# Performance work log

Hardware: AMD Instinct MI355X
Metric: run time of the kernel (lower is better)

Reference implementation:

```python
import jax, jax.numpy as jnp
import numpy as np

B, C, H, W = 16, 16, 256, 256
HID, OUT_C, IN_C = 128, 13, 3

_SOBEL_X = np.array([[-1, 0, 1], [-2, 0, 2], [-1, 0, 1]], dtype=np.float32)
_SOBEL_Y = _SOBEL_X.T


def setup_inputs() -> dict:
    key = jax.random.key(0)
    k1, k2, k3, k4 = jax.random.split(key, 4)
    return {
        "input_grid": jax.random.normal(k1, (B, C, H, W), dtype=jnp.float32),
        "w1": jax.random.normal(k2, (HID, 3 * C), dtype=jnp.float32) * 0.0001,
        "b1": jax.random.normal(k3, (HID,), dtype=jnp.float32) * 0.0001,
        "w2": jax.random.normal(k4, (OUT_C, HID), dtype=jnp.float32) * 0.0001,
    }


def _depthwise_sobel(x_padded, filt2d):
    # x_padded: [B, C, H+2, W+2]; depthwise 3x3 valid conv (groups=C)
    c = x_padded.shape[1]
    kern = jnp.broadcast_to(jnp.asarray(filt2d)[None, None], (c, 1, 3, 3))
    return jax.lax.conv_general_dilated(
        x_padded, kern, window_strides=(1, 1), padding="VALID",
        feature_group_count=c,
        dimension_numbers=("NCHW", "OIHW", "NCHW"))


def reference(input_grid, w1, b1, w2):
    # circular pad by 1 on spatial dims
    xp = jnp.pad(input_grid, ((0, 0), (0, 0), (1, 1), (1, 1)), mode="wrap")
    gx = _depthwise_sobel(xp, _SOBEL_X)
    gy = _depthwise_sobel(xp, _SOBEL_Y)
    # perception grid: [B, 3C, H, W]
    perception = jnp.concatenate([input_grid, gx, gy], axis=1)
    # update network: 1x1 conv -> ReLU -> 1x1 conv (dropout = identity in eval)
    h = jax.nn.relu(jnp.einsum("bchw,oc->bohw", perception, w1)
                    + b1[None, :, None, None])
    ds = jnp.einsum("bchw,oc->bohw", h, w2)  # [B, C-IN_C, H, W]
    # residual add to channels 3: of the state
    return input_grid.at[:, IN_C:].add(ds)
```

## Files before the change

### kernel.cpp

```cpp
#include <hip/hip_runtime.h>

#define BB   16
#define CC   16
#define HH   256
#define WW   256
#define HID  128
#define OUTC 13

typedef short short8 __attribute__((ext_vector_type(8)));
typedef float floatx16 __attribute__((ext_vector_type(16)));

__device__ __forceinline__ unsigned short f2bf(float x) {
    unsigned int u = __float_as_uint(x);
    u += 0x7fffu + ((u >> 16) & 1u);
    return (unsigned short)(u >> 16);
}

#define W1F_BYTES 36864
#define W2F_OFF   36864

__global__ __launch_bounds__(256) void gca_prep(
    const float* __restrict__ w1, const float* __restrict__ w2,
    unsigned char* __restrict__ ws)
{
    const int id = blockIdx.x * 256 + threadIdx.x;
    const float SX[9] = {-1.f, 0.f, 1.f, -2.f, 0.f, 2.f, -1.f, 0.f, 1.f};
    const float SY[9] = {-1.f, -2.f, -1.f, 0.f, 0.f, 0.f, 1.f, 2.f, 1.f};

    if (id < 2304) {
        const int mtG  = id / 576;
        const int rem  = id % 576;
        const int tap  = rem / 64;
        const int lane = rem % 64;
        const int p  = lane & 31, hi = lane >> 5;
        const int hid = 32 * mtG + p;
        const float cen = (tap == 4) ? 1.f : 0.f;
        const float sxv = SX[tap], syv = SY[tap];
        const float* wr = w1 + hid * 48;
        unsigned int o[4];
        for (int k = 0; k < 4; ++k) {
            int c0 = 8 * hi + 2 * k;
            float v0 = wr[c0]     * cen + wr[16 + c0]     * sxv + wr[32 + c0]     * syv;
            float v1 = wr[c0 + 1] * cen + wr[16 + c0 + 1] * sxv + wr[32 + c0 + 1] * syv;
            o[k] = (unsigned int)f2bf(v0) | ((unsigned int)f2bf(v1) << 16);
        }
        *(uint4*)(ws + (size_t)id * 16) = make_uint4(o[0], o[1], o[2], o[3]);
    } else if (id < 2816) {
        const int id2 = id - 2304;
        const int s    = id2 / 64;
        const int lane = id2 % 64;
        const int outc = lane & 31, hi = lane >> 5;
        unsigned int o[4];
        for (int k = 0; k < 4; ++k) {
            int hid0 = 16 * s + 8 * hi + 2 * k;
            float v0 = (outc < OUTC) ? w2[outc * HID + hid0]     : 0.f;
            float v1 = (outc < OUTC) ? w2[outc * HID + hid0 + 1] : 0.f;
            o[k] = (unsigned int)f2bf(v0) | ((unsigned int)f2bf(v1) << 16);
        }
        *(uint4*)(ws + W2F_OFF + (size_t)id2 * 16) = make_uint4(o[0], o[1], o[2], o[3]);
    }
}

#define TILE_DW 6120
#define CBUF_DW 2304

__global__ __launch_bounds__(256) void gca_main(
    const float* __restrict__ in,
    const float* __restrict__ b1,
    const unsigned char* __restrict__ ws,
    float* __restrict__ out)
{
    __shared__ unsigned int lds[TILE_DW + CBUF_DW];

    const int tid  = threadIdx.x;
    const int wid  = tid >> 6;
    const int lane = tid & 63;
    const int hw   = wid & 1;
    const int P    = wid >> 1;
    const int p    = lane & 31;
    const int hi   = lane >> 5;

    const int bI = blockIdx.x >> 7;
    const int rm = blockIdx.x & 127;
    const int y0 = (rm >> 3) << 4;
    const int x0 = (rm & 7)  << 5;

    {
        unsigned short* tus = (unsigned short*)lds;
        const float* inb = in + ((size_t)bI << 20);
        for (int i = tid; i < 16 * 18 * 34; i += 256) {
            int c   = i / 612;
            int rem = i % 612;
            int row = rem / 34;
            int col = rem % 34;
            int y = (y0 + row - 1) & 255;
            int x = (x0 + col - 1) & 255;
            float v = inb[(c << 16) + (y << 8) + x];
            tus[(row * 34 + col) * 20 + c] = f2bf(v);
        }
    }
    __syncthreads();

    const unsigned char* w1f = ws + ((size_t)(2 * hw) * 9) * 64 * 16;
    const unsigned char* w2f = ws + W2F_OFF + (size_t)(4 * hw) * 64 * 16;
    const int cb = TILE_DW + P * (64 * 18) + lane * 18;

#pragma unroll 1
    for (int t = 0; t < 8; ++t) {
        const int row = y0 + 2 * t + P;

        floatx16 acc1[2];
#pragma unroll
        for (int m = 0; m < 2; ++m) {
            const int hb = 64 * hw + 32 * m + 4 * hi;
#pragma unroll
            for (int rr = 0; rr < 4; ++rr) {
                float4 bv = *(const float4*)(b1 + hb + 8 * rr);
                acc1[m][4 * rr + 0] = bv.x;
                acc1[m][4 * rr + 1] = bv.y;
                acc1[m][4 * rr + 2] = bv.z;
                acc1[m][4 * rr + 3] = bv.w;
            }
        }

#pragma unroll
        for (int tap = 0; tap < 9; ++tap) {
            const int tr  = 2 * t + P + tap / 3;
            const int col = p + tap % 3;
            const int dwo = (tr * 34 + col) * 10 + 4 * hi;
            union { unsigned int u[4]; short8 s; } bfr;
            uint2 lo2 = *(const uint2*)&lds[dwo];
            uint2 hi2 = *(const uint2*)&lds[dwo + 2];
            bfr.u[0] = lo2.x; bfr.u[1] = lo2.y; bfr.u[2] = hi2.x; bfr.u[3] = hi2.y;
#pragma unroll
            for (int m = 0; m < 2; ++m) {
                short8 af = *(const short8*)(w1f + (size_t)((m * 9 + tap) * 64 + lane) * 16);
                acc1[m] = __builtin_amdgcn_mfma_f32_32x32x16_bf16(af, bfr.s, acc1[m], 0, 0, 0);
            }
        }

        uint2 hrun[8];
#pragma unroll
        for (int m = 0; m < 2; ++m)
#pragma unroll
            for (int rr = 0; rr < 4; ++rr) {
                float h0 = fmaxf(acc1[m][4 * rr + 0], 0.f);
                float h1 = fmaxf(acc1[m][4 * rr + 1], 0.f);
                float h2 = fmaxf(acc1[m][4 * rr + 2], 0.f);
                float h3 = fmaxf(acc1[m][4 * rr + 3], 0.f);
                hrun[4 * m + rr].x = (unsigned int)f2bf(h0) | ((unsigned int)f2bf(h1) << 16);
                hrun[4 * m + rr].y = (unsigned int)f2bf(h2) | ((unsigned int)f2bf(h3) << 16);
            }

        floatx16 acc2 = {};
#pragma unroll
        for (int sp = 0; sp < 4; ++sp) {
            uint2 r0 = hrun[2 * sp];
            uint2 r1 = hrun[2 * sp + 1];
            uint2 x0s, x1s;
            x0s.x = (unsigned int)__shfl_xor((int)r0.x, 32);
            x0s.y = (unsigned int)__shfl_xor((int)r0.y, 32);
            x1s.x = (unsigned int)__shfl_xor((int)r1.x, 32);
            x1s.y = (unsigned int)__shfl_xor((int)r1.y, 32);
            union { unsigned int u[4]; short8 s; } b2;
            uint2 lo = hi ? x1s : r0;
            uint2 hg = hi ? r1  : x0s;
            b2.u[0] = lo.x; b2.u[1] = lo.y; b2.u[2] = hg.x; b2.u[3] = hg.y;
            short8 a2 = *(const short8*)(w2f + (size_t)(sp * 64 + lane) * 16);
            acc2 = __builtin_amdgcn_mfma_f32_32x32x16_bf16(a2, b2.s, acc2, 0, 0, 0);
        }

        if (hw == 1) {
#pragma unroll
            for (int k = 0; k < 8; ++k) {
                uint2 v;
                v.x = __float_as_uint(acc2[2 * k]);
                v.y = __float_as_uint(acc2[2 * k + 1]);
                *(uint2*)&lds[cb + 2 * k] = v;
            }
        }
        __syncthreads();

        if (hw == 0) {
#pragma unroll
            for (int r = 0; r < 16; ++r) {
                int outc = (r & 3) + 8 * (r >> 2) + 4 * hi;
                if (outc < OUTC) {
                    float sum = acc2[r] + __uint_as_float(lds[cb + r]);
                    int idx = ((bI * 16 + 3 + outc) << 16) + (row << 8) + x0 + p;
                    out[idx] = in[idx] + sum;
                }
            }
        } else {
#pragma unroll
            for (int k = 0; k < 2; ++k) {
                int e = lane + 64 * k;
                if (e < 96) {
                    int c  = e >> 5;
                    int px = e & 31;
                    int idx = ((bI * 16 + c) << 16) + (row << 8) + x0 + px;
                    out[idx] = in[idx];
                }
            }
        }
        __syncthreads();
    }
}

extern "C" void kernel_launch(void* const* d_in, const int* in_sizes, int n_in,
                              void* d_out, int out_size, void* d_ws, size_t ws_size,
                              hipStream_t stream) {
    const float* x  = (const float*)d_in[0];
    const float* w1 = (const float*)d_in[1];
    const float* b1 = (const float*)d_in[2];
    const float* w2 = (const float*)d_in[3];
    float* out = (float*)d_out;
    unsigned char* ws = (unsigned char*)d_ws;

    hipLaunchKernelGGL(gca_prep, dim3(11), dim3(256), 0, stream, w1, w2, ws);
    hipLaunchKernelGGL(gca_main, dim3(2048), dim3(256), 0, stream, x, b1, ws, out);
}
```

Before: 214.2 us.

## Halve block tile to 8 rows with 2 waves and vectorize bf16 tile loading

Each block now handles 8 output rows with 128 threads (two waves, one per hidden half) instead of 16 rows with four waves. This halves LDS per block and doubles the grid, aiming for more resident blocks and better latency hiding. The halo tile load drops its per-element div/mod and 16-bit scattered LDS stores. Instead each thread loads coalesced rows for four channels and writes packed bf16 pairs as 32-bit words. The trade-off is a larger halo fraction (10 loaded rows per 8 output rows) and more per-block setup.

```diff
diff --git a/kernel.cpp b/kernel.cpp
--- a/kernel.cpp
+++ b/kernel.cpp
@@ -14,6 +14,9 @@
     unsigned int u = __float_as_uint(x);
     u += 0x7fffu + ((u >> 16) & 1u);
     return (unsigned short)(u >> 16);
+}
+__device__ __forceinline__ unsigned int pack2(float lo, float hi) {
+    return (unsigned int)f2bf(lo) | ((unsigned int)f2bf(hi) << 16);
 }
 
 #define W1F_BYTES 36864
@@ -61,53 +64,68 @@
     }
 }
 
-#define TILE_DW 6120
-#define CBUF_DW 2304
-
-__global__ __launch_bounds__(256) void gca_main(
+#define TILE_DW 3400
+#define CBUF_DW 1152
+#define LDS_DW  (TILE_DW + CBUF_DW)
+
+__global__ __launch_bounds__(128) void gca_main(
     const float* __restrict__ in,
     const float* __restrict__ b1,
     const unsigned char* __restrict__ ws,
     float* __restrict__ out)
 {
-    __shared__ unsigned int lds[TILE_DW + CBUF_DW];
+    __shared__ unsigned int lds[LDS_DW];
 
     const int tid  = threadIdx.x;
     const int wid  = tid >> 6;
     const int lane = tid & 63;
-    const int hw   = wid & 1;
-    const int P    = wid >> 1;
+    const int hw   = wid;
     const int p    = lane & 31;
     const int hi   = lane >> 5;
 
-    const int bI = blockIdx.x >> 7;
-    const int rm = blockIdx.x & 127;
-    const int y0 = (rm >> 3) << 4;
+    const int bI = blockIdx.x >> 8;
+    const int rm = blockIdx.x & 255;
+    const int y0 = (rm >> 3) << 3;
     const int x0 = (rm & 7)  << 5;
 
+    const float* inb  = in  + ((size_t)bI << 20);
+    float*       outb = out + ((size_t)bI << 20);
+
     {
-        unsigned short* tus = (unsigned short*)lds;
-        const float* inb = in + ((size_t)bI << 20);
-        for (int i = tid; i < 16 * 18 * 34; i += 256) {
-            int c   = i / 612;
-            int rem = i % 612;
-            int row = rem / 34;
-            int col = rem % 34;
-            int y = (y0 + row - 1) & 255;
-            int x = (x0 + col - 1) & 255;
-            float v = inb[(c << 16) + (y << 8) + x];
-            tus[(row * 34 + col) * 20 + c] = f2bf(v);
+        const int g = tid >> 5, l = tid & 31;
+        const float* cp0 = inb + ((size_t)(2 * g) << 16);
+        const int xA = (x0 + l - 1) & 255;
+        const int xB = (x0 + l + 31) & 255;
+        const int ldsA = l * 10 + g;
+        const int ldsB = (l + 32) * 10 + g;
+        const bool doB = (l < 2);
+        for (int rw = 0; rw < 10; ++rw) {
+            const int yo = ((y0 + rw - 1) & 255) << 8;
+            float a0 = cp0[yo + xA];
+            float a1 = cp0[yo + xA + (1 << 16)];
+            float b0 = cp0[yo + xA + (8 << 16)];
+            float b1v = cp0[yo + xA + (9 << 16)];
+            lds[rw * 340 + ldsA]     = pack2(a0, a1);
+            lds[rw * 340 + ldsA + 4] = pack2(b0, b1v);
+            if (doB) {
+                float c0 = cp0[yo + xB];
+                float c1 = cp0[yo + xB + (1 << 16)];
+                float d0 = cp0[yo + xB + (8 << 16)];
+                float d1 = cp0[yo + xB + (9 << 16)];
+                lds[rw * 340 + ldsB]     = pack2(c0, c1);
+                lds[rw * 340 + ldsB + 4] = pack2(d0, d1);
+            }
         }
     }
     __syncthreads();
 
     const unsigned char* w1f = ws + ((size_t)(2 * hw) * 9) * 64 * 16;
     const unsigned char* w2f = ws + W2F_OFF + (size_t)(4 * hw) * 64 * 16;
-    const int cb = TILE_DW + P * (64 * 18) + lane * 18;
+    const int cb = TILE_DW + lane * 18;
 
 #pragma unroll 1
     for (int t = 0; t < 8; ++t) {
-        const int row = y0 + 2 * t + P;
+        const int row = y0 + t;
 
         floatx16 acc1[2];
 #pragma unroll
@@ -125,7 +143,7 @@
 
 #pragma unroll
         for (int tap = 0; tap < 9; ++tap) {
-            const int tr  = 2 * t + P + tap / 3;
+            const int tr  = t + tap / 3;
             const int col = p + tap % 3;
             const int dwo = (tr * 34 + col) * 10 + 4 * hi;
             union { unsigned int u[4]; short8 s; } bfr;
@@ -148,8 +166,8 @@
                 float h1 = fmaxf(acc1[m][4 * rr + 1], 0.f);
                 float h2 = fmaxf(acc1[m][4 * rr + 2], 0.f);
                 float h3 = fmaxf(acc1[m][4 * rr + 3], 0.f);
-                hrun[4 * m + rr].x = (unsigned int)f2bf(h0) | ((unsigned int)f2bf(h1) << 16);
-                hrun[4 * m + rr].y = (unsigned int)f2bf(h2) | ((unsigned int)f2bf(h3) << 16);
+                hrun[4 * m + rr].x = pack2(h0, h1);
+                hrun[4 * m + rr].y = pack2(h2, h3);
             }
 
         floatx16 acc2 = {};
@@ -218,5 +236,5 @@
     unsigned char* ws = (unsigned char*)d_ws;
 
     hipLaunchKernelGGL(gca_prep, dim3(11), dim3(256), 0, stream, w1, w2, ws);
-    hipLaunchKernelGGL(gca_main, dim3(2048), dim3(256), 0, stream, x, b1, ws, out);
-}
+    hipLaunchKernelGGL(gca_main, dim3(4096), dim3(128), 0, stream, x, b1, ws, out);
+}
```

Result: slower. 248.9 us (+16.2%).
